# Kernel optimization log

Measured on AMD Instinct MI355X. Metric: run time of the kernel, lower is better.

Reference implementation:

```python
import jax, jax.numpy as jnp
import numpy as np


def setup_inputs() -> dict:
    key = jax.random.key(0)
    ks = jax.random.split(key, 6)
    B, H, W, C = 4, 64, 64, 256
    D = 256 // 4  # inter_channel // 4
    return {
        "g": jax.random.normal(ks[0], (B, H, W, C), dtype=jnp.float32),
        "x": jax.random.normal(ks[1], (B, H, W, C), dtype=jnp.float32),
        "x_query": jax.random.normal(ks[2], (B, H, W, D), dtype=jnp.float32),
        "phi_g": jax.random.normal(ks[3], (B, H, W, D), dtype=jnp.float32),
        "x_value": jax.random.normal(ks[4], (B, H, W, C), dtype=jnp.float32),
        "k": jax.random.normal(ks[5], (1,), dtype=jnp.float32),
    }


def reference(g, x, x_query, phi_g, x_value, k):
    B, H, W, C = x.shape
    D = x_query.shape[-1]
    HW = H * W
    q = x_query.reshape(B, HW, D)
    pg = phi_g.reshape(B, HW, D)
    v = x_value.reshape(B, HW, C)
    # scale[b,i,j] = sum_d phi_g[b,i,d] * x_query[b,j,d]  -> (B, HW, HW)
    scale = jnp.einsum("bid,bjd->bij", pg, q)
    soft = jax.nn.softmax(scale, axis=-1)
    # scaled_value[b,i,c] = sum_j soft[b,i,j] * v[b,j,c]
    sv = jnp.einsum("bij,bjc->bic", soft, v).reshape(B, H, W, C)
    layero = k * sv + x
    return jnp.concatenate([layero, g], axis=3)
```

## Files before the change

### kernel.cpp

```cpp
#include <hip/hip_runtime.h>

#define N_  4096
#define D_  64
#define C_  256

typedef short bf16x8 __attribute__((ext_vector_type(8)));
typedef float f32x4  __attribute__((ext_vector_type(4)));

#define CHEAP_BARRIER() asm volatile("s_waitcnt lgkmcnt(0)\n\ts_barrier" ::: "memory")

__device__ __forceinline__ unsigned short f2bf(float f) {
    union { float f; unsigned int i; } v; v.f = f;
    unsigned int r = v.i + 0x7fffu + ((v.i >> 16) & 1u);
    return (unsigned short)(r >> 16);
}

__global__ void prepass_kernel(const float* __restrict__ xq,
                               const float* __restrict__ pg,
                               const float* __restrict__ xv,
                               unsigned short* __restrict__ qbf,
                               unsigned short* __restrict__ pgbf,
                               unsigned short* __restrict__ vt2) {
    const int bid = blockIdx.x;
    const int t   = threadIdx.x;
    if (bid < 512) {
        const float* src = (bid < 256) ? xq : pg;
        unsigned short* dst = (bid < 256) ? qbf : pgbf;
        const int base = (bid & 255) * 1024 + t;
#pragma unroll
        for (int it = 0; it < 4; ++it) {
            const int i = base + it * 256;
            float4 v = ((const float4*)src)[i];
            ushort4 o;
            o.x = f2bf(v.x); o.y = f2bf(v.y); o.z = f2bf(v.z); o.w = f2bf(v.w);
            ((ushort4*)dst)[i] = o;
        }
        return;
    }

    __shared__ unsigned short vs[128 * 66];
    const int vb   = bid - 512;
    const int b    = vb >> 7;
    const int rem  = vb & 127;
    const int jt   = rem >> 2;
    const int cq   = rem & 3;
    const int lane = t & 63;
    const int w    = t >> 6;
    const int l15  = lane & 15;
    const int quad = lane >> 4;

    {
        const int jr = t >> 4;
        const int c0 = (t & 15) * 4;
        const float* src = xv + ((size_t)b * N_ + jt * 128 + jr) * C_ + cq * 64 + c0;
        unsigned short* dst = &vs[jr * 66 + c0];
#pragma unroll
        for (int p = 0; p < 8; ++p) {
            const float4 v4 = *(const float4*)(src + (size_t)p * 16 * C_);
            const unsigned int lo = (unsigned)f2bf(v4.x) | ((unsigned)f2bf(v4.y) << 16);
            const unsigned int hi = (unsigned)f2bf(v4.z) | ((unsigned)f2bf(v4.w) << 16);
            *(unsigned int*)(dst + p * 16 * 66)     = lo;
            *(unsigned int*)(dst + p * 16 * 66 + 2) = hi;
        }
    }
    __syncthreads();

    const int ks = w;
#pragma unroll
    for (int cb = 0; cb < 4; ++cb) {
        const unsigned short* pr = &vs[(ks * 32 + quad * 8) * 66 + cb * 16 + l15];
        const unsigned short e0 = pr[0 * 66], e1 = pr[1 * 66];
        const unsigned short e2 = pr[2 * 66], e3 = pr[3 * 66];
        const unsigned short e4 = pr[4 * 66], e5 = pr[5 * 66];
        const unsigned short e6 = pr[6 * 66], e7 = pr[7 * 66];
        uint4 o;
        o.x = (unsigned)e0 | ((unsigned)e1 << 16);
        o.y = (unsigned)e2 | ((unsigned)e3 << 16);
        o.z = (unsigned)e4 | ((unsigned)e5 << 16);
        o.w = (unsigned)e6 | ((unsigned)e7 << 16);
        const int f = ((b * 32 + jt) * 16 + (cq * 4 + cb)) * 4 + ks;
        *(uint4*)(vt2 + (size_t)f * 512 + lane * 8) = o;
    }
}

__global__ __launch_bounds__(512, 2) void attn_main(
    const float* __restrict__ g,  const float* __restrict__ x,
    const float* __restrict__ kk, float* __restrict__ out,
    const unsigned short* __restrict__ qbf,
    const unsigned short* __restrict__ pgbf,
    const unsigned short* __restrict__ vt2)
{
    __shared__ unsigned short p_lds[2][64 * 128];
    __shared__ float s_l[64];

    const int t    = threadIdx.x;
    const int lane = t & 63;
    const int w    = t >> 6;
    const int l15  = lane & 15;
    const int quad = lane >> 4;
    const int swz  = (l15 & 7) << 4;

    const int bid = blockIdx.x;
    const int b   = bid & 3;
    const int rg  = bid >> 2;
    const int i0  = rg * 64;
    const size_t rowbase = (size_t)b * N_ + i0;

    if (t < 64) s_l[t] = 0.f;

#pragma unroll
    for (int it = 0; it < 8; ++it) {
        const int row = it * 8 + w;
        const int c4  = lane * 4;
        const float4 gv = *(const float4*)(g + (rowbase + row) * C_ + c4);
        *(float4*)(out + (rowbase + row) * (2 * C_) + C_ + c4) = gv;
    }

    bf16x8 pgf[4][2];
#pragma unroll
    for (int nt = 0; nt < 4; ++nt)
#pragma unroll
        for (int ks = 0; ks < 2; ++ks)
            pgf[nt][ks] = *(const bf16x8*)(pgbf +
                (rowbase + nt * 16 + l15) * D_ + ks * 32 + quad * 8);

    f32x4 oacc[4][2];
#pragma unroll
    for (int mt = 0; mt < 4; ++mt) { oacc[mt][0] = (f32x4){0.f,0.f,0.f,0.f};
                                     oacc[mt][1] = (f32x4){0.f,0.f,0.f,0.f}; }
    float ls[4] = {0.f, 0.f, 0.f, 0.f};

    const unsigned short* qb  = qbf + (size_t)b * N_ * D_;
    const unsigned short* vtb = vt2 + (size_t)b * N_ * C_;
    unsigned short* const pb0 = &p_lds[0][0];
    unsigned short* const pb1 = &p_lds[1][0];

    auto load_q = [&](bf16x8 (&qf)[2], int jt) {
#pragma unroll
        for (int ks = 0; ks < 2; ++ks)
            qf[ks] = *(const bf16x8*)(qb +
                (size_t)(jt * 128 + w * 16 + l15) * D_ + ks * 32 + quad * 8);
    };
    auto load_v = [&](bf16x8 (&vf)[4][2], int jt) {
        const unsigned short* tbase = vtb + (size_t)jt * 32768;
#pragma unroll
        for (int ks = 0; ks < 4; ++ks)
#pragma unroll
            for (int ctl = 0; ctl < 2; ++ctl)
                vf[ks][ctl] = *(const bf16x8*)(tbase +
                    (size_t)(((w * 2 + ctl) * 4) + ks) * 512 + lane * 8);
    };
    auto s_step = [&](const bf16x8 (&qf)[2], unsigned short* pbuf) {
        f32x4 sacc[4];
#pragma unroll
        for (int nt = 0; nt < 4; ++nt) sacc[nt] = (f32x4){0.f,0.f,0.f,0.f};
#pragma unroll
        for (int ks = 0; ks < 2; ++ks)
#pragma unroll
            for (int nt = 0; nt < 4; ++nt)
                sacc[nt] = __builtin_amdgcn_mfma_f32_16x16x32_bf16(
                    qf[ks], pgf[nt][ks], sacc[nt], 0, 0, 0);
#pragma unroll
        for (int nt = 0; nt < 4; ++nt) {
            const float p0 = __expf(sacc[nt][0]);
            const float p1 = __expf(sacc[nt][1]);
            const float p2 = __expf(sacc[nt][2]);
            const float p3 = __expf(sacc[nt][3]);
            ls[nt] += (p0 + p1) + (p2 + p3);
            ushort4 pk;
            pk.x = f2bf(p0); pk.y = f2bf(p1); pk.z = f2bf(p2); pk.w = f2bf(p3);
            const int wb = ((nt * 16 + l15) * 256 + (w * 16 + quad * 4) * 2) ^ swz;
            *(ushort4*)((char*)pbuf + wb) = pk;
        }
    };
    auto pv_step = [&](const bf16x8 (&vf)[4][2], const unsigned short* pbuf) {
#pragma unroll
        for (int ks = 0; ks < 4; ++ks) {
            bf16x8 pa[4];
#pragma unroll
            for (int mt = 0; mt < 4; ++mt) {
                const int rb = ((mt * 16 + l15) * 256 + (ks * 32 + quad * 8) * 2) ^ swz;
                pa[mt] = *(const bf16x8*)((const char*)pbuf + rb);
            }
#pragma unroll
            for (int mt = 0; mt < 4; ++mt) {
                oacc[mt][0] = __builtin_amdgcn_mfma_f32_16x16x32_bf16(pa[mt], vf[ks][0], oacc[mt][0], 0, 0, 0);
                oacc[mt][1] = __builtin_amdgcn_mfma_f32_16x16x32_bf16(pa[mt], vf[ks][1], oacc[mt][1], 0, 0, 0);
            }
        }
    };

    bf16x8 qfA[2], qfB[2], vfA[4][2], vfB[4][2];

    load_q(qfA, 0);
    load_v(vfA, 0);
    s_step(qfA, pb0);
    load_q(qfB, 1);
    CHEAP_BARRIER();

#pragma unroll 1
    for (int jtp = 0; jtp < 15; ++jtp) {
        const int jt0 = 2 * jtp;
        load_v(vfB, jt0 + 1);
        load_q(qfA, jt0 + 2);
        s_step(qfB, pb1);
        pv_step(vfA, pb0);
        CHEAP_BARRIER();
        load_v(vfA, jt0 + 2);
        load_q(qfB, jt0 + 3);
        s_step(qfA, pb0);
        pv_step(vfB, pb1);
        CHEAP_BARRIER();
    }
    load_v(vfB, 31);
    s_step(qfB, pb1);
    pv_step(vfA, pb0);
    CHEAP_BARRIER();
    pv_step(vfB, pb1);

#pragma unroll
    for (int nt = 0; nt < 4; ++nt) {
        float s = ls[nt];
        s += __shfl_xor(s, 16);
        s += __shfl_xor(s, 32);
        if (lane < 16) atomicAdd(&s_l[nt * 16 + lane], s);
    }
    __syncthreads();

    const float kval = kk[0];
#pragma unroll
    for (int mt = 0; mt < 4; ++mt)
#pragma unroll
        for (int r = 0; r < 4; ++r) {
            const int m = mt * 16 + quad * 4 + r;
            const float linv = 1.f / s_l[m];
            const size_t row = rowbase + m;
#pragma unroll
            for (int ctl = 0; ctl < 2; ++ctl) {
                const int c = w * 32 + ctl * 16 + l15;
                out[row * (2 * C_) + c] = kval * (oacc[mt][ctl][r] * linv) + x[row * C_ + c];
            }
        }
}

#define ROWS 4
#define FNT  256
__global__ __launch_bounds__(FNT, 2) void attn_fallback(
    const float* __restrict__ g, const float* __restrict__ x,
    const float* __restrict__ xq, const float* __restrict__ pg,
    const float* __restrict__ xv, const float* __restrict__ kk,
    float* __restrict__ out)
{
    __shared__ __align__(16) float s_pg[ROWS][D_];
    __shared__ __align__(16) float s_sc[N_ * ROWS];
    __shared__ float s_rmax[4][ROWS];
    __shared__ float s_rsum[4][ROWS];

    const int t = threadIdx.x, lane = t & 63, w = t >> 6, blk = blockIdx.x;
    const int b = blk >> 10, i0 = (blk & 1023) * ROWS;
    const size_t rowbase = (size_t)b * N_ + i0;
    {
        const int r = t >> 6, cc = (t & 63) * 4;
        const float4 gv = *(const float4*)(g + (rowbase + r) * C_ + cc);
        *(float4*)(out + (rowbase + r) * (2 * C_) + C_ + cc) = gv;
    }
    { const int r = t >> 6, d = t & 63; s_pg[r][d] = pg[(rowbase + r) * D_ + d]; }
    __syncthreads();
    const float* qb = xq + (size_t)b * N_ * D_;
    float lmax[ROWS];
#pragma unroll
    for (int r = 0; r < ROWS; ++r) lmax[r] = -1e30f;
    for (int jj = 0; jj < N_ / FNT; ++jj) {
        const int j = t + jj * FNT;
        const float4* q4p = (const float4*)(qb + (size_t)j * D_);
        float s[ROWS] = {0.f, 0.f, 0.f, 0.f};
#pragma unroll
        for (int u = 0; u < D_ / 8; ++u) {
            const float4 qa = q4p[u * 2], qc = q4p[u * 2 + 1];
#pragma unroll
            for (int r = 0; r < ROWS; ++r) {
                const float4 pa = *(const float4*)&s_pg[r][u * 8];
                const float4 pb = *(const float4*)&s_pg[r][u * 8 + 4];
                s[r] += qa.x * pa.x + qa.y * pa.y + qa.z * pa.z + qa.w * pa.w
                      + qc.x * pb.x + qc.y * pb.y + qc.z * pb.z + qc.w * pb.w;
            }
        }
        *(float4*)&s_sc[j * ROWS] = make_float4(s[0], s[1], s[2], s[3]);
#pragma unroll
        for (int r = 0; r < ROWS; ++r) lmax[r] = fmaxf(lmax[r], s[r]);
    }
#pragma unroll
    for (int r = 0; r < ROWS; ++r) {
        float m = lmax[r];
        for (int o = 32; o > 0; o >>= 1) m = fmaxf(m, __shfl_down(m, o));
        if (lane == 0) s_rmax[w][r] = m;
    }
    __syncthreads();
    float bmax[ROWS];
#pragma unroll
    for (int r = 0; r < ROWS; ++r)
        bmax[r] = fmaxf(fmaxf(s_rmax[0][r], s_rmax[1][r]), fmaxf(s_rmax[2][r], s_rmax[3][r]));
    float lsum[ROWS] = {0.f, 0.f, 0.f, 0.f};
    for (int jj = 0; jj < N_ / FNT; ++jj) {
        const int j = t + jj * FNT;
        float4 s4 = *(const float4*)&s_sc[j * ROWS];
        s4.x = __expf(s4.x - bmax[0]); s4.y = __expf(s4.y - bmax[1]);
        s4.z = __expf(s4.z - bmax[2]); s4.w = __expf(s4.w - bmax[3]);
        *(float4*)&s_sc[j * ROWS] = s4;
        lsum[0] += s4.x; lsum[1] += s4.y; lsum[2] += s4.z; lsum[3] += s4.w;
    }
#pragma unroll
    for (int r = 0; r < ROWS; ++r) {
        float sm = lsum[r];
        for (int o = 32; o > 0; o >>= 1) sm += __shfl_down(sm, o);
        if (lane == 0) s_rsum[w][r] = sm;
    }
    __syncthreads();
    float rinv[ROWS];
#pragma unroll
    for (int r = 0; r < ROWS; ++r)
        rinv[r] = 1.f / (s_rsum[0][r] + s_rsum[1][r] + s_rsum[2][r] + s_rsum[3][r]);
    const int jg = lane >> 4;
    const int c0 = (w * 16 + (lane & 15)) * 4;
    const float* vb = xv + (size_t)b * N_ * C_;
    float acc[ROWS][4];
#pragma unroll
    for (int r = 0; r < ROWS; ++r)
#pragma unroll
        for (int q = 0; q < 4; ++q) acc[r][q] = 0.f;
#pragma unroll 4
    for (int jj = 0; jj < N_ / 4; ++jj) {
        const int j = jj * 4 + jg;
        const float4 p4 = *(const float4*)&s_sc[j * ROWS];
        const float4 v4 = *(const float4*)(vb + (size_t)j * C_ + c0);
        acc[0][0] += p4.x * v4.x; acc[0][1] += p4.x * v4.y; acc[0][2] += p4.x * v4.z; acc[0][3] += p4.x * v4.w;
        acc[1][0] += p4.y * v4.x; acc[1][1] += p4.y * v4.y; acc[1][2] += p4.y * v4.z; acc[1][3] += p4.y * v4.w;
        acc[2][0] += p4.z * v4.x; acc[2][1] += p4.z * v4.y; acc[2][2] += p4.z * v4.z; acc[2][3] += p4.z * v4.w;
        acc[3][0] += p4.w * v4.x; acc[3][1] += p4.w * v4.y; acc[3][2] += p4.w * v4.z; acc[3][3] += p4.w * v4.w;
    }
#pragma unroll
    for (int r = 0; r < ROWS; ++r)
#pragma unroll
        for (int q = 0; q < 4; ++q) {
            acc[r][q] += __shfl_xor(acc[r][q], 16);
            acc[r][q] += __shfl_xor(acc[r][q], 32);
        }
    const float kval = kk[0];
    if (lane < 16) {
        const int c = (w * 16 + lane) * 4;
#pragma unroll
        for (int r = 0; r < ROWS; ++r) {
            const float4 xv4 = *(const float4*)(x + (rowbase + r) * C_ + c);
            float4 ov;
            ov.x = kval * (acc[r][0] * rinv[r]) + xv4.x;
            ov.y = kval * (acc[r][1] * rinv[r]) + xv4.y;
            ov.z = kval * (acc[r][2] * rinv[r]) + xv4.z;
            ov.w = kval * (acc[r][3] * rinv[r]) + xv4.w;
            *(float4*)(out + (rowbase + r) * (2 * C_) + c) = ov;
        }
    }
}

extern "C" void kernel_launch(void* const* d_in, const int* in_sizes, int n_in,
                              void* d_out, int out_size, void* d_ws, size_t ws_size,
                              hipStream_t stream) {
    const float* g  = (const float*)d_in[0];
    const float* x  = (const float*)d_in[1];
    const float* xq = (const float*)d_in[2];
    const float* pg = (const float*)d_in[3];
    const float* xv = (const float*)d_in[4];
    const float* kk = (const float*)d_in[5];
    float* out = (float*)d_out;

    const int B = in_sizes[0] / (N_ * C_);
    const size_t qn = (size_t)B * N_ * D_;
    const size_t vn = (size_t)B * N_ * C_;
    const size_t need = (2 * qn + vn) * sizeof(unsigned short);

    if (B != 4 || ws_size < need) {
        attn_fallback<<<dim3(B * (N_ / ROWS)), FNT, 0, stream>>>(g, x, xq, pg, xv, kk, out);
        return;
    }

    unsigned short* qbf  = (unsigned short*)d_ws;
    unsigned short* pgbf = qbf + qn;
    unsigned short* vt2  = pgbf + qn;

    prepass_kernel<<<dim3(512 + B * 128), 256, 0, stream>>>(xq, pg, xv, qbf, pgbf, vt2);
    attn_main<<<dim3(B * (N_ / 64)), 512, 0, stream>>>(g, x, kk, out, qbf, pgbf, vt2);
}
```

Before: 152.0 us.

## Double block to 16 waves and split key tiles across two wave halves

```diff
diff --git a/kernel.cpp b/kernel.cpp
--- a/kernel.cpp
+++ b/kernel.cpp
@@ -83,14 +83,14 @@
     }
 }
 
-__global__ __launch_bounds__(512, 2) void attn_main(
+__global__ __launch_bounds__(1024, 4) void attn_main(
     const float* __restrict__ g,  const float* __restrict__ x,
     const float* __restrict__ kk, float* __restrict__ out,
     const unsigned short* __restrict__ qbf,
     const unsigned short* __restrict__ pgbf,
     const unsigned short* __restrict__ vt2)
 {
-    __shared__ unsigned short p_lds[2][64 * 128];
+    __shared__ __align__(16) unsigned char smem[73728];
     __shared__ float s_l[64];
 
     const int t    = threadIdx.x;
@@ -99,21 +99,21 @@
     const int l15  = lane & 15;
     const int quad = lane >> 4;
     const int swz  = (l15 & 7) << 4;
+    const int h    = w >> 3;
+    const int oct  = w & 7;
 
     const int bid = blockIdx.x;
     const int b   = bid & 3;
     const int rg  = bid >> 2;
-    const int i0  = rg * 64;
-    const size_t rowbase = (size_t)b * N_ + i0;
+    const size_t rowbase = (size_t)b * N_ + rg * 64;
 
     if (t < 64) s_l[t] = 0.f;
 
 #pragma unroll
-    for (int it = 0; it < 8; ++it) {
-        const int row = it * 8 + w;
-        const int c4  = lane * 4;
-        const float4 gv = *(const float4*)(g + (rowbase + row) * C_ + c4);
-        *(float4*)(out + (rowbase + row) * (2 * C_) + C_ + c4) = gv;
+    for (int it = 0; it < 4; ++it) {
+        const int row = it * 16 + w;
+        const float4 gv = *(const float4*)(g + (rowbase + row) * C_ + lane * 4);
+        *(float4*)(out + (rowbase + row) * (2 * C_) + C_ + lane * 4) = gv;
     }
 
     bf16x8 pgf[4][2];
@@ -132,23 +132,24 @@
 
     const unsigned short* qb  = qbf + (size_t)b * N_ * D_;
     const unsigned short* vtb = vt2 + (size_t)b * N_ * C_;
-    unsigned short* const pb0 = &p_lds[0][0];
-    unsigned short* const pb1 = &p_lds[1][0];
-
-    auto load_q = [&](bf16x8 (&qf)[2], int jt) {
+    unsigned short* const pb0 = (unsigned short*)smem;
+    unsigned short* const pb1 = (unsigned short*)(smem + 32768);
+
+    auto load_q = [&](bf16x8 (&qf)[2], int p) {
+        const int pc = (p < 15) ? p : 15;
 #pragma unroll
         for (int ks = 0; ks < 2; ++ks)
             qf[ks] = *(const bf16x8*)(qb +
-                (size_t)(jt * 128 + w * 16 + l15) * D_ + ks * 32 + quad * 8);
+                (size_t)(pc * 256 + w * 16 + l15) * D_ + ks * 32 + quad * 8);
     };
-    auto load_v = [&](bf16x8 (&vf)[4][2], int jt) {
-        const unsigned short* tbase = vtb + (size_t)jt * 32768;
+    auto load_v = [&](bf16x8 (&vf)[4][2], int p) {
+        const unsigned short* tbase = vtb + (size_t)(2 * p + h) * 32768;
 #pragma unroll
         for (int ks = 0; ks < 4; ++ks)
 #pragma unroll
             for (int ctl = 0; ctl < 2; ++ctl)
                 vf[ks][ctl] = *(const bf16x8*)(tbase +
-                    (size_t)(((w * 2 + ctl) * 4) + ks) * 512 + lane * 8);
+                    (size_t)(((oct * 2 + ctl) * 4) + ks) * 512 + lane * 8);
     };
     auto s_step = [&](const bf16x8 (&qf)[2], unsigned short* pbuf) {
         f32x4 sacc[4];
@@ -169,7 +170,7 @@
             ls[nt] += (p0 + p1) + (p2 + p3);
             ushort4 pk;
             pk.x = f2bf(p0); pk.y = f2bf(p1); pk.z = f2bf(p2); pk.w = f2bf(p3);
-            const int wb = ((nt * 16 + l15) * 256 + (w * 16 + quad * 4) * 2) ^ swz;
+            const int wb = ((nt * 16 + l15) * 512 + (w * 16 + quad * 4) * 2) ^ swz;
             *(ushort4*)((char*)pbuf + wb) = pk;
         }
     };
@@ -179,7 +180,7 @@
             bf16x8 pa[4];
 #pragma unroll
             for (int mt = 0; mt < 4; ++mt) {
-                const int rb = ((mt * 16 + l15) * 256 + (ks * 32 + quad * 8) * 2) ^ swz;
+                const int rb = ((mt * 16 + l15) * 512 + h * 256 + ks * 64 + quad * 16) ^ swz;
                 pa[mt] = *(const bf16x8*)((const char*)pbuf + rb);
             }
 #pragma unroll
@@ -199,20 +200,20 @@
     CHEAP_BARRIER();
 
 #pragma unroll 1
-    for (int jtp = 0; jtp < 15; ++jtp) {
-        const int jt0 = 2 * jtp;
-        load_v(vfB, jt0 + 1);
-        load_q(qfA, jt0 + 2);
+    for (int pp = 0; pp < 7; ++pp) {
+        const int p = 2 * pp;
+        load_v(vfB, p + 1);
+        load_q(qfA, p + 2);
         s_step(qfB, pb1);
         pv_step(vfA, pb0);
         CHEAP_BARRIER();
-        load_v(vfA, jt0 + 2);
-        load_q(qfB, jt0 + 3);
+        load_v(vfA, p + 2);
+        load_q(qfB, p + 3);
         s_step(qfA, pb0);
         pv_step(vfB, pb1);
         CHEAP_BARRIER();
     }
-    load_v(vfB, 31);
+    load_v(vfB, 15);
     s_step(qfB, pb1);
     pv_step(vfA, pb0);
     CHEAP_BARRIER();
@@ -227,20 +228,34 @@
     }
     __syncthreads();
 
-    const float kval = kk[0];
-#pragma unroll
-    for (int mt = 0; mt < 4; ++mt)
-#pragma unroll
-        for (int r = 0; r < 4; ++r) {
-            const int m = mt * 16 + quad * 4 + r;
-            const float linv = 1.f / s_l[m];
-            const size_t row = rowbase + m;
-#pragma unroll
-            for (int ctl = 0; ctl < 2; ++ctl) {
-                const int c = w * 32 + ctl * 16 + l15;
-                out[row * (2 * C_) + c] = kval * (oacc[mt][ctl][r] * linv) + x[row * C_ + c];
+    float* Rg = (float*)(smem + (size_t)oct * 9216);
+    if (h == 1) {
+#pragma unroll
+        for (int mt = 0; mt < 4; ++mt)
+#pragma unroll
+            for (int ctl = 0; ctl < 2; ++ctl)
+#pragma unroll
+                for (int r = 0; r < 4; ++r)
+                    Rg[(mt * 16 + quad * 4 + r) * 36 + ctl * 16 + l15] = oacc[mt][ctl][r];
+    }
+    __syncthreads();
+    if (h == 0) {
+        const float kval = kk[0];
+#pragma unroll
+        for (int mt = 0; mt < 4; ++mt)
+#pragma unroll
+            for (int r = 0; r < 4; ++r) {
+                const int m = mt * 16 + quad * 4 + r;
+                const float linv = 1.f / s_l[m];
+                const size_t row = rowbase + m;
+#pragma unroll
+                for (int ctl = 0; ctl < 2; ++ctl) {
+                    const int c = oct * 32 + ctl * 16 + l15;
+                    const float sum = oacc[mt][ctl][r] + Rg[m * 36 + ctl * 16 + l15];
+                    out[row * (2 * C_) + c] = kval * (sum * linv) + x[row * C_ + c];
+                }
             }
-        }
+    }
 }
 
 #define ROWS 4
@@ -387,5 +402,5 @@
     unsigned short* vt2  = pgbf + qn;
 
     prepass_kernel<<<dim3(512 + B * 128), 256, 0, stream>>>(xq, pg, xv, qbf, pgbf, vt2);
-    attn_main<<<dim3(B * (N_ / 64)), 512, 0, stream>>>(g, x, kk, out, qbf, pgbf, vt2);
+    attn_main<<<dim3(B * (N_ / 64)), 1024, 0, stream>>>(g, x, kk, out, qbf, pgbf, vt2);
 }
```

Result: slower. 264.0 us (+73.7%).
